# Performance work log

Measured on AMD Instinct MI355X. Metric: run time of the kernel, lower is better.

The kernel has to match this reference:

```python
import jax, jax.numpy as jnp
import numpy as np

B, C, LF = 64, 256, 32
H = W = LF  # required: H = W = att_dilation*(LF-1)+1 with att_dilation=1
C1 = 256    # conv1_outchannel


def setup_inputs() -> dict:
    key = jax.random.key(0)
    k0, k1, k2 = jax.random.split(key, 3)
    x = jax.random.normal(k0, (B, C, H, W), jnp.float32)
    conv1_w = jax.random.normal(k1, (C1, C, 7, 7), jnp.float32) * 0.02
    conv1_b = jnp.zeros((C1,), jnp.float32)
    bn1_g = jnp.ones((C1,), jnp.float32)
    bn1_b = jnp.zeros((C1,), jnp.float32)
    conv2_w = jax.random.normal(k2, (LF * LF, C1, 1, 1), jnp.float32) * 0.02
    conv2_b = jnp.zeros((LF * LF,), jnp.float32)
    bn2_g = jnp.ones((LF * LF,), jnp.float32)
    bn2_b = jnp.zeros((LF * LF,), jnp.float32)
    return {"x": x, "conv1_w": conv1_w, "conv1_b": conv1_b, "bn1_g": bn1_g,
            "bn1_b": bn1_b, "conv2_w": conv2_w, "conv2_b": conv2_b,
            "bn2_g": bn2_g, "bn2_b": bn2_b}


def _bn(h, g, b, eps=1e-5):
    # training-mode BatchNorm2d: biased batch stats over (N,H,W)
    m = h.mean(axis=(0, 2, 3), keepdims=True)
    v = jnp.var(h, axis=(0, 2, 3), keepdims=True)
    return g[None, :, None, None] * (h - m) * jax.lax.rsqrt(v + eps) + b[None, :, None, None]


def reference(x, conv1_w, conv1_b, bn1_g, bn1_b, conv2_w, conv2_b, bn2_g, bn2_b):
    dn = ('NCHW', 'OIHW', 'NCHW')
    # conv1: 7x7, dilation 2, 'same' padding (=6)
    h = jax.lax.conv_general_dilated(x, conv1_w, (1, 1), ((6, 6), (6, 6)),
                                     rhs_dilation=(2, 2), dimension_numbers=dn)
    h = _bn(h + conv1_b[None, :, None, None], bn1_g, bn1_b)
    # conv_last: 1x1 -> LF^2 channels
    k = jax.lax.conv_general_dilated(h, conv2_w, (1, 1), ((0, 0), (0, 0)),
                                     dimension_numbers=dn)
    k = _bn(k + conv2_b[None, :, None, None], bn2_g, bn2_b)
    k = jax.nn.softmax(k, axis=1)                 # [B, LF*LF, H, W]
    kmap = k.reshape(B, LF, LF, H, W)             # per-pixel LFxLF window weights
    # conv3d-with-groups=B hack == per-pixel weighted sum over the whole LFxLF map:
    # y[b,i,j,c] = sum_{u,v} kmap[b,u,v,i,j] * x[b,c,u,v]
    y = jnp.einsum('buvij,bcuv->bijc', kmap, x)   # [B, H, W, C]
    # torch.reshape of [1, B*H*W, C, 1, 1] to (B, C, H, W): raw row-major reinterpret
    return y.reshape(B, C, H, W)
```

## Files before the change

kernel.cpp:

```cpp
#include <hip/hip_runtime.h>

typedef unsigned short u16;
typedef unsigned int u32;
typedef short bf16x8 __attribute__((ext_vector_type(8)));
typedef float f32x4 __attribute__((ext_vector_type(4)));

#define NB   64
#define NC   256
#define NO   256
#define NM   1024
#define PW   44
#define PPIX 1936

__device__ __forceinline__ u16 f2bf(float f) {
    u32 u = __builtin_bit_cast(u32, f);
    u32 r = (u + 0x7FFFu + ((u >> 16) & 1u)) >> 16;
    return (u16)r;
}
__device__ __forceinline__ float bf2f(u32 lo16) {
    return __builtin_bit_cast(float, lo16 << 16);
}
__device__ __forceinline__ void ld16(const void* g, void* l) {
    __builtin_amdgcn_global_load_lds((const __attribute__((address_space(1))) u32*)g,
                                     (__attribute__((address_space(3))) u32*)l, 16, 0, 0);
}

#define VMCNT(n) { asm volatile("s_waitcnt vmcnt(" #n ")" ::: "memory"); __builtin_amdgcn_sched_barrier(0); }
#define LGKM(n)  { asm volatile("s_waitcnt lgkmcnt(" #n ")" ::: "memory"); __builtin_amdgcn_sched_barrier(0); }

__global__ __launch_bounds__(256) void k_transpose_pad(const float* __restrict__ x, u16* __restrict__ xp) {
    __shared__ u16 tile[64 * 65];
    const int b = blockIdx.z, ij0 = blockIdx.x * 64, c0 = blockIdx.y * 64;
    const int tid = threadIdx.x;
#pragma unroll
    for (int it = 0; it < 16; ++it) {
        int idx = it * 256 + tid;
        int cr = idx >> 6, ijr = idx & 63;
        tile[ijr * 65 + cr] = f2bf(x[((size_t)(b * NC + c0 + cr) << 10) + ij0 + ijr]);
    }
    __syncthreads();
#pragma unroll
    for (int it = 0; it < 16; ++it) {
        int idx = it * 256 + tid;
        int ijr = idx >> 6, cr = idx & 63;
        int pix = ij0 + ijr;
        int i = pix >> 5, j = pix & 31;
        int prow = (i + 6) * PW + (j + 6);
        xp[((size_t)(b * PPIX + prow) << 8) + c0 + cr] = tile[ijr * 65 + cr];
    }
}

__global__ __launch_bounds__(256) void k_w1prep(const float* __restrict__ w1, u16* __restrict__ w1t) {
    const int o = blockIdx.x, c = threadIdx.x;
    const float* src = w1 + ((size_t)(o * NC + c)) * 49;
#pragma unroll
    for (int t = 0; t < 49; ++t)
        w1t[((size_t)(t * NO + o) << 8) + c] = f2bf(src[t]);
}

__global__ __launch_bounds__(512, 1) void k_conv1(const u16* __restrict__ xp, const u16* __restrict__ w1t,
                                                  u16* __restrict__ h, float* __restrict__ s1, float* __restrict__ q1) {
    __shared__ u16 lsA[4 * 256 * 32];
    __shared__ u16 lsB[4 * 256 * 32];
    const int tid = threadIdx.x, wv = tid >> 6, lane = tid & 63;
    const int wm = wv & 1, wn = wv >> 1;
    const int bb = blockIdx.z, ij0 = blockIdx.x * 256;

    f32x4 acc[8][4] = {};
    bf16x8 aX[8], bX[4], aY[8], bY[4];

    const int lc8 = (((tid & 3) ^ ((tid >> 3) & 3)) << 3);
    int aRow[2], bRow[2], dstO[2];
#pragma unroll
    for (int c = 0; c < 2; ++c) {
        int r = (c << 7) + (tid >> 2);
        int pix = ij0 + r, i = pix >> 5, j = pix & 31;
        aRow[c] = ((bb * PPIX + i * PW + j) << 8) + lc8;
        bRow[c] = (r << 8) + lc8;
        dstO[c] = ((c << 7) + (wv << 4)) << 5;
    }
    const int chsw = (((lane >> 4) ^ (((lane & 15) >> 1) & 3)) << 3);
    const u16* pA0 = lsA + (((wm << 7) + (lane & 15)) << 5) + chsw;
    const u16* pB0 = lsB + (((wn << 6) + (lane & 15)) << 5) + chsw;

    int sp = 0, sq = 0, stap = 0, sci = 0, skh = 0, sreg = 0;
    auto STAGE = [&]() {
        const int toff = (((sp << 1) * PW + (sq << 1)) << 8) + (sci << 6) + (skh << 5);
        const int woff = (stap << 16) + (sci << 6) + (skh << 5);
        u16* dA = (u16*)lsA + (sreg << 13);
        u16* dB = (u16*)lsB + (sreg << 13);
#pragma unroll
        for (int c = 0; c < 2; ++c) ld16(xp + aRow[c] + toff, dA + dstO[c]);
#pragma unroll
        for (int c = 0; c < 2; ++c) ld16(w1t + bRow[c] + woff, dB + dstO[c]);
        sreg = (sreg + 1) & 3;
        skh ^= 1;
        if (!skh) {
            ++stap; ++sq;
            if (sq == 7) { sq = 0; ++sp; }
            if (stap == 49) { stap = 0; sp = 0; sq = 0; ++sci; }
        }
    };
    auto RD = [&](int v, bf16x8 (&a)[8], bf16x8 (&b)[4]) {
        const int rb = (v & 3) << 13;
        const u16* pA = pA0 + rb;
        const u16* pB = pB0 + rb;
#pragma unroll
        for (int fi = 0; fi < 8; ++fi) a[fi] = *(const bf16x8*)(pA + (fi << 9));
#pragma unroll
        for (int fj = 0; fj < 4; ++fj) b[fj] = *(const bf16x8*)(pB + (fj << 9));
    };
    auto MM = [&](bf16x8 (&a)[8], bf16x8 (&b)[4]) {
        __builtin_amdgcn_s_setprio(1);
#pragma unroll
        for (int fi = 0; fi < 8; ++fi)
#pragma unroll
            for (int fj = 0; fj < 4; ++fj)
                acc[fi][fj] = __builtin_amdgcn_mfma_f32_16x16x32_bf16(a[fi], b[fj], acc[fi][fj], 0, 0, 0);
        __builtin_amdgcn_s_setprio(0);
    };

    STAGE(); STAGE(); STAGE();
    VMCNT(8);
    __builtin_amdgcn_s_barrier();
    RD(0, aX, bX);

#pragma unroll 1
    for (int u = 0; u < 388; u += 2) {
        VMCNT(4);
        __builtin_amdgcn_s_barrier();
        RD(u + 1, aY, bY);
        STAGE();
        LGKM(12);
        MM(aX, bX);

        VMCNT(4);
        __builtin_amdgcn_s_barrier();
        RD(u + 2, aX, bX);
        STAGE();
        LGKM(12);
        MM(aY, bY);
    }
    VMCNT(4);
    __builtin_amdgcn_s_barrier();
    RD(389, aY, bY);
    STAGE();
    LGKM(12);
    MM(aX, bX);

    VMCNT(4);
    __builtin_amdgcn_s_barrier();
    RD(390, aX, bX);
    LGKM(12);
    MM(aY, bY);

    VMCNT(0);
    __builtin_amdgcn_s_barrier();
    RD(391, aY, bY);
    LGKM(12);
    MM(aX, bX);

    LGKM(0);
    MM(aY, bY);

    const int colb = (wn << 6) + (lane & 15);
    const int rowb = ij0 + (wm << 7) + ((lane >> 4) << 2);
#pragma unroll
    for (int fj = 0; fj < 4; ++fj) {
        const int col = colb + (fj << 4);
        float s = 0.f, qq = 0.f;
#pragma unroll
        for (int fi = 0; fi < 8; ++fi) {
            const int row = rowb + (fi << 4);
#pragma unroll
            for (int v = 0; v < 4; ++v) {
                float val = acc[fi][fj][v];
                h[((size_t)((bb << 10) + row + v) << 8) + col] = f2bf(val);
                s += val; qq += val * val;
            }
        }
        s += __shfl_xor(s, 16);  s += __shfl_xor(s, 32);
        qq += __shfl_xor(qq, 16); qq += __shfl_xor(qq, 32);
        if (lane < 16) { atomicAdd(&s1[col], s); atomicAdd(&q1[col], qq); }
    }
}

__global__ __launch_bounds__(256) void k_fold2(const float* __restrict__ w2,
                                               const float* __restrict__ s1, const float* __restrict__ q1,
                                               const float* __restrict__ g1, u16* __restrict__ w2s) {
    const int m = blockIdx.x, c = threadIdx.x;
    float mean = s1[c] * (1.f / 65536.f);
    float var  = fmaxf(q1[c] * (1.f / 65536.f) - mean * mean, 0.f);
    float a1   = g1[c] * rsqrtf(var + 1e-5f);
    size_t idx = ((size_t)m << 8) + c;
    w2s[idx] = f2bf(w2[idx] * a1);
}

__global__ __launch_bounds__(512, 1) void k_conv2(const u16* __restrict__ h, const u16* __restrict__ w2s,
                                                  u16* __restrict__ kb, float* __restrict__ s2, float* __restrict__ q2) {
    __shared__ u16 lsA[4 * 256 * 32];
    __shared__ u16 lsB[4 * 256 * 32];
    const int tid = threadIdx.x, wv = tid >> 6, lane = tid & 63;
    const int wm = wv & 1, wn = wv >> 1;
    const int bid = blockIdx.x;
    const int bb = bid & 63, r2 = bid >> 6;
    const int ij0 = (r2 >> 2) << 8, m0 = (r2 & 3) << 8;

    f32x4 acc[8][4] = {};
    bf16x8 aX[8], bX[4], aY[8], bY[4];

    const int lc8 = (((tid & 3) ^ ((tid >> 3) & 3)) << 3);
    int aRow[2], bRow[2], dstO[2];
#pragma unroll
    for (int c = 0; c < 2; ++c) {
        int rr = (c << 7) + (tid >> 2);
        aRow[c] = (((bb << 10) + ij0 + rr) << 8) + lc8;
        bRow[c] = ((m0 + rr) << 8) + lc8;
        dstO[c] = ((c << 7) + (wv << 4)) << 5;
    }
    const int chsw = (((lane >> 4) ^ (((lane & 15) >> 1) & 3)) << 3);
    const u16* pA0 = lsA + (((wm << 7) + (lane & 15)) << 5) + chsw;
    const u16* pB0 = lsB + (((wn << 6) + (lane & 15)) << 5) + chsw;

    int sk = 0, sreg = 0;
    auto STAGE = [&]() {
        const int off = sk << 5;
        u16* dA = (u16*)lsA + (sreg << 13);
        u16* dB = (u16*)lsB + (sreg << 13);
#pragma unroll
        for (int c = 0; c < 2; ++c) ld16(h + aRow[c] + off, dA + dstO[c]);
#pragma unroll
        for (int c = 0; c < 2; ++c) ld16(w2s + bRow[c] + off, dB + dstO[c]);
        sreg = (sreg + 1) & 3;
        ++sk;
    };
    auto RD = [&](int v, bf16x8 (&a)[8], bf16x8 (&b)[4]) {
        const int rb = (v & 3) << 13;
        const u16* pA = pA0 + rb;
        const u16* pB = pB0 + rb;
#pragma unroll
        for (int fi = 0; fi < 8; ++fi) a[fi] = *(const bf16x8*)(pA + (fi << 9));
#pragma unroll
        for (int fj = 0; fj < 4; ++fj) b[fj] = *(const bf16x8*)(pB + (fj << 9));
    };
    auto MM = [&](bf16x8 (&a)[8], bf16x8 (&b)[4]) {
        __builtin_amdgcn_s_setprio(1);
#pragma unroll
        for (int fi = 0; fi < 8; ++fi)
#pragma unroll
            for (int fj = 0; fj < 4; ++fj)
                acc[fi][fj] = __builtin_amdgcn_mfma_f32_16x16x32_bf16(a[fi], b[fj], acc[fi][fj], 0, 0, 0);
        __builtin_amdgcn_s_setprio(0);
    };

    STAGE(); STAGE(); STAGE();
    VMCNT(8);
    __builtin_amdgcn_s_barrier();
    RD(0, aX, bX);

#pragma unroll 1
    for (int u = 0; u < 4; u += 2) {
        VMCNT(4);
        __builtin_amdgcn_s_barrier();
        RD(u + 1, aY, bY);
        STAGE();
        LGKM(12);
        MM(aX, bX);

        VMCNT(4);
        __builtin_amdgcn_s_barrier();
        RD(u + 2, aX, bX);
        STAGE();
        LGKM(12);
        MM(aY, bY);
    }
    VMCNT(4);
    __builtin_amdgcn_s_barrier();
    RD(5, aY, bY);
    STAGE();
    LGKM(12);
    MM(aX, bX);

    VMCNT(4);
    __builtin_amdgcn_s_barrier();
    RD(6, aX, bX);
    LGKM(12);
    MM(aY, bY);

    VMCNT(0);
    __builtin_amdgcn_s_barrier();
    RD(7, aY, bY);
    LGKM(12);
    MM(aX, bX);

    LGKM(0);
    MM(aY, bY);

    const int colb = m0 + (wn << 6) + (lane & 15);
    const int rowb = ij0 + (wm << 7) + ((lane >> 4) << 2);
#pragma unroll
    for (int fj = 0; fj < 4; ++fj) {
        const int col = colb + (fj << 4);
        float s = 0.f, qq = 0.f;
#pragma unroll
        for (int fi = 0; fi < 8; ++fi) {
            const int row = rowb + (fi << 4);
#pragma unroll
            for (int v = 0; v < 4; ++v) {
                float val = acc[fi][fj][v];
                kb[((size_t)((bb << 10) + row + v) << 10) + col] = f2bf(val);
                s += val; qq += val * val;
            }
        }
        s += __shfl_xor(s, 16);  s += __shfl_xor(s, 32);
        qq += __shfl_xor(qq, 16); qq += __shfl_xor(qq, 32);
        if (lane < 16) { atomicAdd(&s2[col], s); atomicAdd(&q2[col], qq); }
    }
}

__global__ void k_bn2fin(const float* __restrict__ s2, const float* __restrict__ q2,
                         const float* __restrict__ g2, const float* __restrict__ b2,
                         float* __restrict__ a2, float* __restrict__ b2f) {
    const int m = blockIdx.x * 256 + threadIdx.x;
    float mean = s2[m] * (1.f / 65536.f);
    float var  = fmaxf(q2[m] * (1.f / 65536.f) - mean * mean, 0.f);
    float a = g2[m] * rsqrtf(var + 1e-5f);
    a2[m] = a;
    b2f[m] = b2[m] - mean * a;
}

__global__ __launch_bounds__(256) void k_rowstat(const u16* __restrict__ kb,
                                                 const float* __restrict__ a2, const float* __restrict__ b2f,
                                                 float* __restrict__ rowmx, float* __restrict__ rowinv) {
    const int tid = threadIdx.x, lane = tid & 63, wv = tid >> 6;
    const int m0 = lane << 4;
    float av[16], bv[16];
#pragma unroll
    for (int i = 0; i < 16; i += 4) {
        *(float4*)(av + i) = *(const float4*)(a2 + m0 + i);
        *(float4*)(bv + i) = *(const float4*)(b2f + m0 + i);
    }
    const int rbase = (blockIdx.x << 5) + (wv << 3);
#pragma unroll 1
    for (int r = 0; r < 8; ++r) {
        const int row = rbase + r;
        const u16* p = kb + ((size_t)row << 10) + m0;
        uint4 v0 = *(const uint4*)p;
        uint4 v1 = *(const uint4*)(p + 8);
        float u[16];
        u[0]  = bf2f(v0.x & 0xFFFFu); u[1]  = __builtin_bit_cast(float, v0.x & 0xFFFF0000u);
        u[2]  = bf2f(v0.y & 0xFFFFu); u[3]  = __builtin_bit_cast(float, v0.y & 0xFFFF0000u);
        u[4]  = bf2f(v0.z & 0xFFFFu); u[5]  = __builtin_bit_cast(float, v0.z & 0xFFFF0000u);
        u[6]  = bf2f(v0.w & 0xFFFFu); u[7]  = __builtin_bit_cast(float, v0.w & 0xFFFF0000u);
        u[8]  = bf2f(v1.x & 0xFFFFu); u[9]  = __builtin_bit_cast(float, v1.x & 0xFFFF0000u);
        u[10] = bf2f(v1.y & 0xFFFFu); u[11] = __builtin_bit_cast(float, v1.y & 0xFFFF0000u);
        u[12] = bf2f(v1.z & 0xFFFFu); u[13] = __builtin_bit_cast(float, v1.z & 0xFFFF0000u);
        u[14] = bf2f(v1.w & 0xFFFFu); u[15] = __builtin_bit_cast(float, v1.w & 0xFFFF0000u);
#pragma unroll
        for (int i = 0; i < 16; ++i) u[i] = av[i] * u[i] + bv[i];
        float mx = u[0];
#pragma unroll
        for (int i = 1; i < 16; ++i) mx = fmaxf(mx, u[i]);
#pragma unroll
        for (int off = 32; off; off >>= 1) mx = fmaxf(mx, __shfl_xor(mx, off));
        float s = 0.f;
#pragma unroll
        for (int i = 0; i < 16; ++i) s += __expf(u[i] - mx);
#pragma unroll
        for (int off = 32; off; off >>= 1) s += __shfl_xor(s, off);
        if (lane == 0) { rowmx[row] = mx; rowinv[row] = 1.f / s; }
    }
}

__global__ __launch_bounds__(512, 2) void k_final(const u16* __restrict__ kb, const float* __restrict__ x,
                                                  const float* __restrict__ a2, const float* __restrict__ b2f,
                                                  const float* __restrict__ rowmx, const float* __restrict__ rowinv,
                                                  float* __restrict__ out) {
    __shared__ u16 lsA[128 * 32];
    __shared__ u16 lsB[256 * 32];
    const int tid = threadIdx.x, wv = tid >> 6, lane = tid & 63;
    const int wm = wv >> 2, wn = wv & 3;
    const int bid = blockIdx.x;
    const int bb = bid & 63, ij0 = (bid >> 6) << 7;

    f32x4 acc[4][4] = {};

    const int ar = tid >> 2, am8 = (tid & 3) << 3;
    const size_t aGlb = (((size_t)((bb << 10) + ij0 + ar)) << 10) + am8;
    u16* aLds = (u16*)lsA + (ar << 5) + (((tid & 3) ^ ((ar >> 1) & 3)) << 3);
    const float mxr = rowmx[(bb << 10) + ij0 + ar];
    const float invr = rowinv[(bb << 10) + ij0 + ar];
    const int br = tid >> 1, bm16 = (tid & 1) << 4;
    const size_t bGlb = (((size_t)((bb << 8) + br)) << 10) + bm16;
    const int bswz = (br >> 1) & 3;
    u16* bLds0 = (u16*)lsB + (br << 5) + (((((tid & 1) << 1) | 0) ^ bswz) << 3);
    u16* bLds1 = (u16*)lsB + (br << 5) + (((((tid & 1) << 1) | 1) ^ bswz) << 3);
    const int chsw = (((lane >> 4) ^ (((lane & 15) >> 1) & 3)) << 3);
    const u16* pA0 = lsA + (((wm << 6) + (lane & 15)) << 5) + chsw;
    const u16* pB0 = lsB + (((wn << 6) + (lane & 15)) << 5) + chsw;

#pragma unroll 1
    for (int s = 0; s < 32; ++s) {
        const int cc = s << 5;
        uint4 av = *(const uint4*)(kb + aGlb + cc);
        float4 xb0 = *(const float4*)(x + bGlb + cc);
        float4 xb1 = *(const float4*)(x + bGlb + cc + 4);
        float4 xb2 = *(const float4*)(x + bGlb + cc + 8);
        float4 xb3 = *(const float4*)(x + bGlb + cc + 12);
        float4 a2lo = *(const float4*)(a2 + cc + am8);
        float4 a2hi = *(const float4*)(a2 + cc + am8 + 4);
        float4 bflo = *(const float4*)(b2f + cc + am8);
        float4 bfhi = *(const float4*)(b2f + cc + am8 + 4);
        float va[8];
        va[0] = bf2f(av.x & 0xFFFFu); va[1] = __builtin_bit_cast(float, av.x & 0xFFFF0000u);
        va[2] = bf2f(av.y & 0xFFFFu); va[3] = __builtin_bit_cast(float, av.y & 0xFFFF0000u);
        va[4] = bf2f(av.z & 0xFFFFu); va[5] = __builtin_bit_cast(float, av.z & 0xFFFF0000u);
        va[6] = bf2f(av.w & 0xFFFFu); va[7] = __builtin_bit_cast(float, av.w & 0xFFFF0000u);
        float p[8];
        p[0] = __expf(a2lo.x * va[0] + bflo.x - mxr) * invr;
        p[1] = __expf(a2lo.y * va[1] + bflo.y - mxr) * invr;
        p[2] = __expf(a2lo.z * va[2] + bflo.z - mxr) * invr;
        p[3] = __expf(a2lo.w * va[3] + bflo.w - mxr) * invr;
        p[4] = __expf(a2hi.x * va[4] + bfhi.x - mxr) * invr;
        p[5] = __expf(a2hi.y * va[5] + bfhi.y - mxr) * invr;
        p[6] = __expf(a2hi.z * va[6] + bfhi.z - mxr) * invr;
        p[7] = __expf(a2hi.w * va[7] + bfhi.w - mxr) * invr;
        uint4 pa;
        pa.x = (u32)f2bf(p[0]) | ((u32)f2bf(p[1]) << 16);
        pa.y = (u32)f2bf(p[2]) | ((u32)f2bf(p[3]) << 16);
        pa.z = (u32)f2bf(p[4]) | ((u32)f2bf(p[5]) << 16);
        pa.w = (u32)f2bf(p[6]) | ((u32)f2bf(p[7]) << 16);
        uint4 pb0, pb1;
        pb0.x = (u32)f2bf(xb0.x) | ((u32)f2bf(xb0.y) << 16);
        pb0.y = (u32)f2bf(xb0.z) | ((u32)f2bf(xb0.w) << 16);
        pb0.z = (u32)f2bf(xb1.x) | ((u32)f2bf(xb1.y) << 16);
        pb0.w = (u32)f2bf(xb1.z) | ((u32)f2bf(xb1.w) << 16);
        pb1.x = (u32)f2bf(xb2.x) | ((u32)f2bf(xb2.y) << 16);
        pb1.y = (u32)f2bf(xb2.z) | ((u32)f2bf(xb2.w) << 16);
        pb1.z = (u32)f2bf(xb3.x) | ((u32)f2bf(xb3.y) << 16);
        pb1.w = (u32)f2bf(xb3.z) | ((u32)f2bf(xb3.w) << 16);
        __syncthreads();
        *(uint4*)aLds = pa;
        *(uint4*)bLds0 = pb0;
        *(uint4*)bLds1 = pb1;
        __syncthreads();
        bf16x8 af[4], bv[4];
#pragma unroll
        for (int f = 0; f < 4; ++f) af[f] = *(const bf16x8*)(pA0 + (f << 9));
#pragma unroll
        for (int f = 0; f < 4; ++f) bv[f] = *(const bf16x8*)(pB0 + (f << 9));
#pragma unroll
        for (int fi = 0; fi < 4; ++fi)
#pragma unroll
            for (int fj = 0; fj < 4; ++fj)
                acc[fi][fj] = __builtin_amdgcn_mfma_f32_16x16x32_bf16(af[fi], bv[fj], acc[fi][fj], 0, 0, 0);
    }
    const int colb = (wn << 6) + (lane & 15);
    const int rowb = ij0 + (wm << 6) + ((lane >> 4) << 2);
#pragma unroll
    for (int fi = 0; fi < 4; ++fi) {
        const int row = rowb + (fi << 4);
#pragma unroll
        for (int fj = 0; fj < 4; ++fj) {
            const int col = colb + (fj << 4);
#pragma unroll
            for (int v = 0; v < 4; ++v)
                out[((size_t)((bb << 10) + row + v) << 8) + col] = acc[fi][fj][v];
        }
    }
}

extern "C" void kernel_launch(void* const* d_in, const int* in_sizes, int n_in,
                              void* d_out, int out_size, void* d_ws, size_t ws_size,
                              hipStream_t stream) {
    const float* x  = (const float*)d_in[0];
    const float* w1 = (const float*)d_in[1];
    const float* g1 = (const float*)d_in[3];
    const float* w2 = (const float*)d_in[5];
    const float* g2 = (const float*)d_in[7];
    const float* b2 = (const float*)d_in[8];
    float* out = (float*)d_out;
    char* ws = (char*)d_ws;

    u16* xp  = (u16*)ws;
    u16* kb  = (u16*)ws;
    u16* h   = (u16*)(ws + 134217728);
    float* rowmx  = (float*)(ws + 134217728);
    float* rowinv = rowmx + 65536;
    u16* w1t = (u16*)(ws + 134217728 + 33554432);
    u16* w2s = w1t;
    char* sm = ws + 134217728 + 33554432 + 6422528;
    float* s1  = (float*)(sm);
    float* q1  = (float*)(sm + 1024);
    float* s2  = (float*)(sm + 2048);
    float* q2  = (float*)(sm + 6144);
    float* a2  = (float*)(sm + 14336);
    float* b2f = (float*)(sm + 18432);

    hipMemsetAsync(sm, 0, 10240, stream);
    hipMemsetAsync(xp, 0, (size_t)NB * PPIX * 256 * 2, stream);
    k_transpose_pad<<<dim3(16, 4, NB), 256, 0, stream>>>(x, xp);
    k_w1prep<<<dim3(256), 256, 0, stream>>>(w1, w1t);
    k_conv1<<<dim3(4, 1, NB), 512, 0, stream>>>(xp, w1t, h, s1, q1);
    k_fold2<<<dim3(1024), 256, 0, stream>>>(w2, s1, q1, g1, w2s);
    k_conv2<<<dim3(1024), 512, 0, stream>>>(h, w2s, kb, s2, q2);
    k_bn2fin<<<dim3(4), 256, 0, stream>>>(s2, q2, g2, b2, a2, b2f);
    k_rowstat<<<dim3(2048), 256, 0, stream>>>(kb, a2, b2f, rowmx, rowinv);
    k_final<<<dim3(512), 512, 0, stream>>>(kb, x, a2, b2f, rowmx, rowinv, out);
}
```

Before: 669.5 us.

## Restructure conv1 GEMM pipeline to double-buffered two-k-half stages per barrier

Replaces the 4-slot ring pipeline, which staged one 32-wide k-half per step with three stages in flight, by a double buffer that stages both k-halves of a tap per iteration. Each iteration waits for all outstanding loads, then reads both halves and runs two MFMA batches, halving the number of barriers. The cost is a shallower prefetch depth: VMCNT(0) each iteration means global loads get only one compute step to hide latency instead of several.

```diff
diff --git a/kernel.cpp b/kernel.cpp
--- a/kernel.cpp
+++ b/kernel.cpp
@@ -83,26 +83,27 @@
     const u16* pA0 = lsA + (((wm << 7) + (lane & 15)) << 5) + chsw;
     const u16* pB0 = lsB + (((wn << 6) + (lane & 15)) << 5) + chsw;
 
-    int sp = 0, sq = 0, stap = 0, sci = 0, skh = 0, sreg = 0;
+    int sp = 0, sq = 0, stap = 0, sci = 0, sbuf = 0;
     auto STAGE = [&]() {
-        const int toff = (((sp << 1) * PW + (sq << 1)) << 8) + (sci << 6) + (skh << 5);
-        const int woff = (stap << 16) + (sci << 6) + (skh << 5);
-        u16* dA = (u16*)lsA + (sreg << 13);
-        u16* dB = (u16*)lsB + (sreg << 13);
-#pragma unroll
-        for (int c = 0; c < 2; ++c) ld16(xp + aRow[c] + toff, dA + dstO[c]);
-#pragma unroll
-        for (int c = 0; c < 2; ++c) ld16(w1t + bRow[c] + woff, dB + dstO[c]);
-        sreg = (sreg + 1) & 3;
-        skh ^= 1;
-        if (!skh) {
-            ++stap; ++sq;
-            if (sq == 7) { sq = 0; ++sp; }
-            if (stap == 49) { stap = 0; sp = 0; sq = 0; ++sci; }
+        const int tbase = (((sp << 1) * PW + (sq << 1)) << 8) + (sci << 6);
+        const int wbase = (stap << 16) + (sci << 6);
+#pragma unroll
+        for (int kh = 0; kh < 2; ++kh) {
+            u16* dA = (u16*)lsA + (((sbuf << 1) | kh) << 13);
+            u16* dB = (u16*)lsB + (((sbuf << 1) | kh) << 13);
+            const int o = kh << 5;
+#pragma unroll
+            for (int c = 0; c < 2; ++c) ld16(xp + aRow[c] + tbase + o, dA + dstO[c]);
+#pragma unroll
+            for (int c = 0; c < 2; ++c) ld16(w1t + bRow[c] + wbase + o, dB + dstO[c]);
         }
+        sbuf ^= 1;
+        ++stap; ++sq;
+        if (sq == 7) { sq = 0; ++sp; }
+        if (stap == 49) { stap = 0; sp = 0; sq = 0; ++sci; }
     };
     auto RD = [&](int v, bf16x8 (&a)[8], bf16x8 (&b)[4]) {
-        const int rb = (v & 3) << 13;
+        const int rb = v << 13;
         const u16* pA = pA0 + rb;
         const u16* pB = pB0 + rb;
 #pragma unroll
@@ -120,48 +121,22 @@
         __builtin_amdgcn_s_setprio(0);
     };
 
-    STAGE(); STAGE(); STAGE();
-    VMCNT(8);
-    __builtin_amdgcn_s_barrier();
-    RD(0, aX, bX);
+    STAGE();
 
 #pragma unroll 1
-    for (int u = 0; u < 388; u += 2) {
-        VMCNT(4);
+    for (int j = 0; j < 196; ++j) {
+        const int p = j & 1;
+        VMCNT(0);
         __builtin_amdgcn_s_barrier();
-        RD(u + 1, aY, bY);
-        STAGE();
+        __builtin_amdgcn_sched_barrier(0);
+        RD(p << 1, aX, bX);
+        RD((p << 1) | 1, aY, bY);
+        if (j < 195) STAGE();
         LGKM(12);
         MM(aX, bX);
-
-        VMCNT(4);
-        __builtin_amdgcn_s_barrier();
-        RD(u + 2, aX, bX);
-        STAGE();
-        LGKM(12);
+        LGKM(0);
         MM(aY, bY);
     }
-    VMCNT(4);
-    __builtin_amdgcn_s_barrier();
-    RD(389, aY, bY);
-    STAGE();
-    LGKM(12);
-    MM(aX, bX);
-
-    VMCNT(4);
-    __builtin_amdgcn_s_barrier();
-    RD(390, aX, bX);
-    LGKM(12);
-    MM(aY, bY);
-
-    VMCNT(0);
-    __builtin_amdgcn_s_barrier();
-    RD(391, aY, bY);
-    LGKM(12);
-    MM(aX, bX);
-
-    LGKM(0);
-    MM(aY, bY);
 
     const int colb = (wn << 6) + (lane & 15);
     const int rowb = ij0 + (wm << 7) + ((lane >> 4) << 2);
```

New measurement: 644.1 us. 3.8% less time.
